# Performance work log

Measured on AMD Instinct MI355X. Metric: run time of the kernel, lower is better.

Reference implementation:

```python
import jax, jax.numpy as jnp
import numpy as np

B, T, N, DIN, DR, DH, K = 8, 40, 1024, 16, 64, 64, 3
DT = 0.05
N_EULER = 2  # Euler sub-steps per observation interval (time_points per step)


def dconv(A, x, W, b):
    feats = [x]
    h = x
    for _ in range(K - 1):
        h = jnp.einsum('bnm,bmd->bnd', A, h)
        feats.append(h)
    return jnp.concatenate(feats, -1) @ W + b


def dcgru(x, h, A, Wg, bg, Wc, bc):
    g = jax.nn.sigmoid(dconv(A, jnp.concatenate([x, h], -1), Wg, bg))
    r, u = jnp.split(g, 2, -1)
    c = jnp.tanh(dconv(A, jnp.concatenate([x, r * h], -1), Wc, bc))
    return u * h + (1.0 - u) * c


def ode_f(h, A, W0, b0, Wout, bout):
    return jnp.tanh(jnp.tanh(dconv(A, h, W0, b0)) @ Wout + bout)


def setup_inputs() -> dict:
    key = jax.random.key(0)
    ks = jax.random.split(key, 32)
    p = lambda k, s: 0.1 * jax.random.normal(k, s, dtype=jnp.float32)
    values = jax.random.normal(ks[0], (B, T, N, DIN), dtype=jnp.float32)
    masks = (jax.random.uniform(ks[1], (B, T, N, DIN)) > 0.3).astype(jnp.float32)
    u = jax.random.uniform(ks[2], (B, N, N), dtype=jnp.float32)
    A = u / u.sum(-1, keepdims=True)  # row-normalized dense diffusion matrix
    d = dict(values=values, masks=masks, A=A,
             h0=p(ks[3], (1, 1, DR)) * 0.1, z0=p(ks[4], (1, 1, DR)) * 0.1,
             gV_Wg=p(ks[5], ((DIN + DR) * K, 2 * DR)), gV_bg=jnp.zeros((2 * DR,)),
             gV_Wc=p(ks[6], ((DIN + DR) * K, DR)), gV_bc=jnp.zeros((DR,)),
             gG_Wg=p(ks[7], ((DIN + DR) * K, 2 * DR)), gG_bg=jnp.zeros((2 * DR,)),
             gG_Wc=p(ks[8], ((DIN + DR) * K, DR)), gG_bc=jnp.zeros((DR,)),
             oV_W0=p(ks[9], (DR * K, DH)), oV_b0=jnp.zeros((DH,)),
             oV_Wout=p(ks[10], (DH, DR)), oV_bout=jnp.zeros((DR,)),
             oG_W0=p(ks[11], (DR * K, DH)), oG_b0=jnp.zeros((DH,)),
             oG_Wout=p(ks[12], (DH, DR)), oG_bout=jnp.zeros((DR,)),
             Wz1=p(ks[13], (DR, DR)), bz1=jnp.zeros((DR,)),
             Wz2=p(ks[14], (DR, DR)), bz2=jnp.zeros((DR,)),
             Wz3=p(ks[15], (DR, DR)), bz3=jnp.zeros((DR,)),
             Wo=p(ks[16], (DR, DIN)), bo=jnp.zeros((DIN,)))
    return d


def reference(values, masks, A, h0, z0,
              gV_Wg, gV_bg, gV_Wc, gV_bc, gG_Wg, gG_bg, gG_Wc, gG_bc,
              oV_W0, oV_b0, oV_Wout, oV_bout, oG_W0, oG_b0, oG_Wout, oG_bout,
              Wz1, bz1, Wz2, bz2, Wz3, bz3, Wo, bo):
    X = values * masks  # [B,T,N,DIN]
    obs = (jnp.abs(masks).sum(-1, keepdims=True) > 1e-4).astype(values.dtype)  # [B,T,N,1]
    hv = jnp.broadcast_to(h0, (B, N, DR))
    zv = jnp.broadcast_to(z0, (B, N, DR))
    dt = DT / N_EULER

    def step(carry, inp):
        hv, zv = carry
        x, m = inp  # [B,N,DIN], [B,N,1]
        for _ in range(N_EULER):  # Euler ODE integration over the interval
            hv = hv + dt * ode_f(hv, A, oV_W0, oV_b0, oV_Wout, oV_bout)
            zv = zv + dt * ode_f(zv, A, oG_W0, oG_b0, oG_Wout, oG_bout)
        hv1, zv1 = hv, zv
        hv2 = dcgru(x, hv1, A, gV_Wg, gV_bg, gV_Wc, gV_bc)
        zv2 = dcgru(x, zv1, A, gG_Wg, gG_bg, gG_Wc, gG_bc)
        hv_new = hv1 * (1.0 - m) + hv2 * m
        zv_new = zv1 * (1.0 - m) + zv2 * m
        return (hv_new, zv_new), (hv1, zv1, hv_new)

    xs = (jnp.swapaxes(X, 0, 1), jnp.swapaxes(obs, 0, 1))  # time-major
    _, (hv_pre, zv_pre, hv_post) = jax.lax.scan(step, (hv, zv), xs)
    hv_pre = jnp.swapaxes(hv_pre, 0, 1)   # [B,T,N,DR]
    zv_pre = jnp.swapaxes(zv_pre, 0, 1)
    gate = jax.nn.sigmoid(jnp.tanh(jnp.tanh(zv_pre @ Wz1 + bz1) @ Wz2 + bz2) @ Wz3 + bz3)
    X_pred = (hv_pre * gate) @ Wo + bo
    return X_pred[:, 1:, :, :]
```

## Files before the change

### kernel.cpp

```cpp
#include <hip/hip_runtime.h>
#include <math.h>


#define T_ 40

typedef __attribute__((ext_vector_type(8))) short short8;
typedef __attribute__((ext_vector_type(4))) float f32x4;

__device__ __forceinline__ float sigm(float x) { return 1.0f / (1.0f + expf(-x)); }

__device__ __forceinline__ unsigned short bfrnd(float x) {
  union { float f; unsigned int u; } v; v.f = x;
  unsigned int u = v.u + 0x7fffu + ((v.u >> 16) & 1u);
  return (unsigned short)(u >> 16);
}
__device__ __forceinline__ unsigned int pk2(float a, float b) {
  return (unsigned int)bfrnd(a) | ((unsigned int)bfrnd(b) << 16);
}

__global__ __launch_bounds__(256) void k_init(float* __restrict__ S, unsigned short* __restrict__ SB,
                                              const float* __restrict__ h0,
                                              const float* __restrict__ z0) {
  int idx = blockIdx.x * 256 + threadIdx.x;
  int c = idx & 63;
  float v = (idx < (8192 * 64)) ? h0[c] : z0[c];
  S[idx] = v;
  int cc = (idx >> 10) & 63;
  float v2 = ((idx >> 16) < 8) ? h0[cc] : z0[cc];
  SB[idx] = bfrnd(v2);
}

__global__ __launch_bounds__(256) void k_asA(const float* __restrict__ A, unsigned short* __restrict__ AS) {
  size_t j = ((size_t)blockIdx.x * 256 + threadIdx.x) * 8;
  if (j >= (size_t)8 * 1024 * 1024) return;
  int b = (int)(j >> 20);
  size_t rem = j & 1048575;
  int r = (int)(rem >> 10), k = (int)(rem & 1023);
  const float* src = A + ((size_t)b << 20) + (size_t)r * 1024 + k;
  float4 v0 = *(const float4*)src;
  float4 v1 = *(const float4*)(src + 4);
  uint4 o;
  o.x = pk2(v0.x, v0.y); o.y = pk2(v0.z, v0.w);
  o.z = pk2(v1.x, v1.y); o.w = pk2(v1.z, v1.w);
  *(uint4*)(AS + ((size_t)b * 2048 + r) * 1024 + k) = o;
}

__global__ __launch_bounds__(256) void k_xb(const float* __restrict__ values,
                                            const float* __restrict__ masks,
                                            unsigned short* __restrict__ XB) {
  const int bt = blockIdx.x;
  const int n0 = blockIdx.y * 256;
  __shared__ float Ls[256][17];
  const int tid = threadIdx.x;
  size_t base = ((size_t)bt * 1024 + n0 + tid) * 16;
#pragma unroll
  for (int c4 = 0; c4 < 4; ++c4) {
    float4 v = *(const float4*)&values[base + c4 * 4];
    float4 m = *(const float4*)&masks[base + c4 * 4];
    Ls[tid][c4 * 4 + 0] = v.x * m.x; Ls[tid][c4 * 4 + 1] = v.y * m.y;
// ... 30 lines not shown

  for (int k0 = 0; k0 < 1024; k0 += 8) {
    int mm = threadIdx.x >> 1, k4 = (threadIdx.x & 1) * 4;
    float4 va = *(const float4*)&Ab[(size_t)(m0 + mm) * 1024 + k0 + k4];
    As[k4 + 0][mm] = va.x; As[k4 + 1][mm] = va.y; As[k4 + 2][mm] = va.z; As[k4 + 3][mm] = va.w;
    int kk = threadIdx.x >> 5, nn = (threadIdx.x & 31) * 4;
    float4 vb = *(const float4*)&Ab[(size_t)(k0 + kk) * 1024 + n0 + nn];
    *(float4*)&Bs[kk][nn] = vb;
    __syncthreads();
#pragma unroll
    for (int k = 0; k < 8; ++k) {
      float a[8], bb[8];
      *(float4*)&a[0] = *(float4*)&As[k][ty * 8];
      *(float4*)&a[4] = *(float4*)&As[k][ty * 8 + 4];
      *(float4*)&bb[0] = *(float4*)&Bs[k][tx * 8];
      *(float4*)&bb[4] = *(float4*)&Bs[k][tx * 8 + 4];
#pragma unroll
      for (int m = 0; m < 8; ++m)
#pragma unroll
        for (int n = 0; n < 8; ++n) acc[m][n] += a[m] * bb[n];
    }
    __syncthreads();
  }
#pragma unroll
  for (int m = 0; m < 8; ++m) {
    unsigned short* C = AS + ((size_t)b * 2048 + 1024 + m0 + ty * 8 + m) * 1024 + n0 + tx * 8;
    uint4 o;
    o.x = pk2(acc[m][0], acc[m][1]); o.y = pk2(acc[m][2], acc[m][3]);
    o.z = pk2(acc[m][4], acc[m][5]); o.w = pk2(acc[m][6], acc[m][7]);
    *(uint4*)C = o;
  }
}

template <int NT, int MODE>
__global__ __launch_bounds__(256) void k_hop_mfma(
    const unsigned short* __restrict__ AS,
    const unsigned short* __restrict__ XB,
    const unsigned short* __restrict__ SB,
    const unsigned short* __restrict__ RHB,
    float* __restrict__ HHS, float* __restrict__ HHX, int t) {
  __shared__ __align__(16) unsigned short lds_a[2][4][512];
  __shared__ __align__(16) unsigned short lds_b[2][NT][512];
  const int tid = threadIdx.x;
  const int w = tid >> 6, l = tid & 63;
  const int b = blockIdx.y;
  const int m0 = blockIdx.x * 64;
  const int lr = l & 15, lk = l >> 4;

  const unsigned short* agp = AS + ((size_t)b * 2048 + m0 + w * 16 + lr) * 1024 + lk * 8;

  const int bstart = (NT == 9) ? ((w == 0) ? 0 : (1 + 2 * w)) : (2 * w);
  const int bcnt   = (NT == 9) ? ((w == 0) ? 3 : 2) : 2;

  auto bsrc = [&](int ct) -> const unsigned short* {
    if (MODE == 1) {
      if (ct == 0)      return XB + (((size_t)(b * T_ + t)) * 16 + lr) * 1024;
      else if (ct < 5)  return SB + ((size_t)b * 64 + (size_t)(ct - 1) * 16 + lr) * 1024;
      else              return SB + ((size_t)(8 + b) * 64 + (size_t)(ct - 5) * 16 + lr) * 1024;
    } else {
      const unsigned short* base = (MODE == 2) ? RHB : SB;
      if (ct < 4) return base + ((size_t)b * 64 + (size_t)ct * 16 + lr) * 1024;
      else        return base + ((size_t)(8 + b) * 64 + (size_t)(ct - 4) * 16 + lr) * 1024;
    }
  };

  f32x4 acc[4][3];
#pragma unroll
  for (int rt = 0; rt < 4; ++rt)
#pragma unroll
    for (int ci = 0; ci < 3; ++ci) acc[rt][ci] = (f32x4){0.f, 0.f, 0.f, 0.f};

#define STAGE(BUF, K0)                                                                         \
  {                                                                                            \
    __builtin_amdgcn_global_load_lds(                                                          \
        (const __attribute__((address_space(1))) void*)(agp + (K0)),                           \
        (__attribute__((address_space(3))) void*)&lds_a[BUF][w][0], 16, 0, 0);                 \
    for (int ct = w; ct < NT; ct += 4)                                                         \
      __builtin_amdgcn_global_load_lds(                                                        \
          (const __attribute__((address_space(1))) void*)(bsrc(ct) + (K0) + lk * 8),           \
          (__attribute__((address_space(3))) void*)&lds_b[BUF][ct][0], 16, 0, 0);              \
  }

  int cur = 0;
  STAGE(0, 0)
  __syncthreads();
  for (int step = 0; step < 32; ++step) {
    const int nxt = cur ^ 1;
    if (step < 31) STAGE(nxt, (step + 1) * 32)
    short8 af[4];
#pragma unroll
    for (int rt = 0; rt < 4; ++rt)
      af[rt] = *(const short8*)&lds_a[cur][rt][l * 8];
#pragma unroll
    for (int ci = 0; ci < 3; ++ci) {
      if (ci < bcnt) {
        short8 bf = *(const short8*)&lds_b[cur][bstart + ci][l * 8];
#pragma unroll
        for (int rt = 0; rt < 4; ++rt)
          acc[rt][ci] = __builtin_amdgcn_mfma_f32_16x16x32_bf16(af[rt], bf, acc[rt][ci], 0, 0, 0);
      }
    }
    __syncthreads();
    cur = nxt;
  }
#undef STAGE

#pragma unroll
  for (int ci = 0; ci < 3; ++ci) {
    if (ci < bcnt) {
      const int ct = bstart + ci;
      float* dst; int ldc, csub;
      if (MODE == 1) {
        if (ct == 0)     { dst = HHX + (size_t)b * 2048 * 16;      ldc = 16; csub = lr; }
        else if (ct < 5) { dst = HHS + (size_t)b * 2048 * 64;      ldc = 64; csub = (ct - 1) * 16 + lr; }
        else             { dst = HHS + (size_t)(8 + b) * 2048 * 64; ldc = 64; csub = (ct - 5) * 16 + lr; }
      } else {
        if (ct < 4) { dst = HHS + (size_t)b * 2048 * 64;       ldc = 64; csub = ct * 16 + lr; }
        else        { dst = HHS + (size_t)(8 + b) * 2048 * 64; ldc = 64; csub = (ct - 4) * 16 + lr; }
      }
#pragma unroll
      for (int rt = 0; rt < 4; ++rt) {
        const int rbase = m0 + rt * 16 + lk * 4;
#pragma unroll
        for (int j = 0; j < 4; ++j)
          dst[(size_t)(rbase + j) * ldc + csub] = acc[rt][ci][j];
      }
    }
  }
}

__global__ __launch_bounds__(256) void k_ode_tail(float* __restrict__ S, unsigned short* __restrict__ SB,
    const float* __restrict__ HHS,
    const float* __restrict__ vW0, const float* __restrict__ vb0,
    const float* __restrict__ vWout, const float* __restrict__ vbout,
    const float* __restrict__ gW0, const float* __restrict__ gb0,
    const float* __restrict__ gWout, const float* __restrict__ gbout) {
  __shared__ float Fs[32][200];
  __shared__ float T1s[32][68];
  __shared__ float Wc[64][64];
  __shared__ float bias[64];
  __shared__ float Ts[64][33];
  const int rowbase = blockIdx.x * 32;
  const int i = rowbase >> 10, st = i >> 3;
  const float* W0 = st ? gW0 : vW0;
  const float* b0 = st ? gb0 : vb0;
  const float* Wo = st ? gWout : vWout;
  const float* bo = st ? gbout : vbout;
  const int r = threadIdx.x >> 3, q = threadIdx.x & 7;

  for (int idx = threadIdx.x; idx < 32 * 64; idx += 256) {
    int rr = idx >> 6, c = idx & 63;
    size_t g = (size_t)(rowbase + rr);
    int n = (int)(g & 1023);
    Fs[rr][c] = S[g * 64 + c];
    Fs[rr][64 + c]  = HHS[((size_t)i * 2048 + n) * 64 + c];
    Fs[rr][128 + c] = HHS[((size_t)i * 2048 + 1024 + n) * 64 + c];
  }
  if (threadIdx.x < 64) bias[threadIdx.x] = b0[threadIdx.x];

  float acc[8];
#pragma unroll
  for (int j = 0; j < 8; ++j) acc[j] = 0.0f;
  for (int kc = 0; kc < 3; ++kc) {
    __syncthreads();
    for (int idx = threadIdx.x; idx < 1024; idx += 256)
      ((float4*)Wc)[idx] = ((const float4*)W0)[kc * 1024 + idx];
    __syncthreads();
#pragma unroll 8
    for (int k = 0; k < 64; ++k) {
      float f = Fs[r][kc * 64 + k];
      float4 w0 = *(float4*)&Wc[k][q * 8];
      float4 w1 = *(float4*)&Wc[k][q * 8 + 4];
      acc[0] += f * w0.x; acc[1] += f * w0.y; acc[2] += f * w0.z; acc[3] += f * w0.w;
      acc[4] += f * w1.x; acc[5] += f * w1.y; acc[6] += f * w1.z; acc[7] += f * w1.w;
    }
  }
#pragma unroll
  for (int j = 0; j < 8; ++j) T1s[r][q * 8 + j] = tanhf(acc[j] + bias[q * 8 + j]);
  __syncthreads();
  if (threadIdx.x < 64) bias[threadIdx.x] = bo[threadIdx.x];
  for (int idx = threadIdx.x; idx < 1024; idx += 256)
    ((float4*)Wc)[idx] = ((const float4*)Wo)[idx];
  __syncthreads();
  float a2[8];
#pragma unroll
  for (int j = 0; j < 8; ++j) a2[j] = 0.0f;
#pragma unroll 8
  for (int k = 0; k < 64; ++k) {
    float f = T1s[r][k];
    float4 w0 = *(float4*)&Wc[k][q * 8];
    float4 w1 = *(float4*)&Wc[k][q * 8 + 4];
    a2[0] += f * w0.x; a2[1] += f * w0.y; a2[2] += f * w0.z; a2[3] += f * w0.w;
    a2[4] += f * w1.x; a2[5] += f * w1.y; a2[6] += f * w1.z; a2[7] += f * w1.w;
  }
  size_t g = (size_t)(rowbase + r);
#pragma unroll
  for (int j = 0; j < 8; ++j) {
    size_t o = g * 64 + q * 8 + j;
    float ns = S[o] + 0.025f * tanhf(a2[j] + bias[q * 8 + j]);
    S[o] = ns;
    Ts[q * 8 + j][r] = ns;
  }
  __syncthreads();
  {
    const int c = threadIdx.x >> 2, p = threadIdx.x & 3;
    const int n0 = rowbase & 1023;
    uint4 o;
    o.x = pk2(Ts[c][p * 8 + 0], Ts[c][p * 8 + 1]);
    o.y = pk2(Ts[c][p * 8 + 2], Ts[c][p * 8 + 3]);
    o.z = pk2(Ts[c][p * 8 + 4], Ts[c][p * 8 + 5]);
    o.w = pk2(Ts[c][p * 8 + 6], Ts[c][p * 8 + 7]);
    *(uint4*)(SB + ((size_t)i * 64 + c) * 1024 + n0 + p * 8) = o;
  }
}

__global__ __launch_bounds__(256) void k_gate_tail(const float* __restrict__ values,
    const float* __restrict__ masks, const float* __restrict__ S,
    const float* __restrict__ HHS, const float* __restrict__ HHX,
    float* __restrict__ RH, unsigned short* __restrict__ RHB, float* __restrict__ U,
    const float* __restrict__ vWg, const float* __restrict__ vbg,
    const float* __restrict__ gWg, const float* __restrict__ gbg, int t) {
  __shared__ float Fs[32][248];
  __shared__ float Wc[48][128];
  __shared__ float bgs[128];
  __shared__ float Ts[64][33];
  const int rowbase = blockIdx.x * 32;
  const int i = rowbase >> 10, st = i >> 3, b = i & 7;
  const float* Wg = st ? gWg : vWg;
  const float* bg = st ? gbg : vbg;
  const int r = threadIdx.x >> 3, q = threadIdx.x & 7;

  for (int idx = threadIdx.x; idx < 32 * 80; idx += 256) {
    int rr = idx / 80, c = idx - rr * 80;
    size_t g = (size_t)(rowbase + rr);
    int n = (int)(g & 1023);
    float xh, v1, v2;
    if (c < 16) {
      size_t xo = ((((size_t)b * T_ + t) << 10) + n) * 16 + c;
      xh = values[xo] * masks[xo];
      v1 = HHX[((size_t)b * 2048 + n) * 16 + c];
      v2 = HHX[((size_t)b * 2048 + 1024 + n) * 16 + c];
    } else {
      xh = S[g * 64 + (c - 16)];
      v1 = HHS[((size_t)i * 2048 + n) * 64 + (c - 16)];
      v2 = HHS[((size_t)i * 2048 + 1024 + n) * 64 + (c - 16)];
    }
    Fs[rr][c] = xh;
    Fs[rr][80 + c]  = v1;
    Fs[rr][160 + c] = v2;
  }
  if (threadIdx.x < 128) bgs[threadIdx.x] = bg[threadIdx.x];

  float acc[16];
#pragma unroll
  for (int j = 0; j < 16; ++j) acc[j] = 0.0f;
  for (int kc = 0; kc < 5; ++kc) {
    __syncthreads();
    for (int idx = threadIdx.x; idx < 1536; idx += 256)
      ((float4*)Wc)[idx] = ((const float4*)Wg)[kc * 1536 + idx];
    __syncthreads();
#pragma unroll 8
    for (int k = 0; k < 48; ++k) {
      float f = Fs[r][kc * 48 + k];
      float4 w0 = *(float4*)&Wc[k][q * 16];
      float4 w1 = *(float4*)&Wc[k][q * 16 + 4];
      float4 w2 = *(float4*)&Wc[k][q * 16 + 8];
      float4 w3 = *(float4*)&Wc[k][q * 16 + 12];
      acc[0]  += f * w0.x; acc[1]  += f * w0.y; acc[2]  += f * w0.z; acc[3]  += f * w0.w;
      acc[4]  += f * w1.x; acc[5]  += f * w1.y; acc[6]  += f * w1.z; acc[7]  += f * w1.w;
      acc[8]  += f * w2.x; acc[9]  += f * w2.y; acc[10] += f * w2.z; acc[11] += f * w2.w;
      acc[12] += f * w3.x; acc[13] += f * w3.y; acc[14] += f * w3.z; acc[15] += f * w3.w;
    }
  }
  size_t g = (size_t)(rowbase + r);
  if (q < 4) {
#pragma unroll
    for (int jj = 0; jj < 16; ++jj) {
      int c = q * 16 + jj;
      float rr_ = sigm(acc[jj] + bgs[c]);
      float rhv = rr_ * Fs[r][16 + c];
      RH[g * 64 + c] = rhv;
      Ts[c][r] = rhv;
    }
  } else {
#pragma unroll
    for (int jj = 0; jj < 16; ++jj) {
      int c = (q - 4) * 16 + jj;
      U[g * 64 + c] = sigm(acc[jj] + bgs[64 + c]);
    }
  }
  __syncthreads();
  {
    const int c = threadIdx.x >> 2, p = threadIdx.x & 3;
    const int n0 = rowbase & 1023;
    uint4 o;
    o.x = pk2(Ts[c][p * 8 + 0], Ts[c][p * 8 + 1]);
    o.y = pk2(Ts[c][p * 8 + 2], Ts[c][p * 8 + 3]);
    o.z = pk2(Ts[c][p * 8 + 4], Ts[c][p * 8 + 5]);
    o.w = pk2(Ts[c][p * 8 + 6], Ts[c][p * 8 + 7]);
    *(uint4*)(RHB + ((size_t)i * 64 + c) * 1024 + n0 + p * 8) = o;
  }
}

__global__ __launch_bounds__(256) void k_cand_tail(const float* __restrict__ values,
    const float* __restrict__ masks, float* __restrict__ S, unsigned short* __restrict__ SB,
    const float* __restrict__ HHS, const float* __restrict__ HHX,
    const float* __restrict__ RH, const float* __restrict__ U,
    const float* __restrict__ vWc, const float* __restrict__ vbc,
    const float* __restrict__ gWc, const float* __restrict__ gbc, int t) {
  __shared__ float Fs[32][248];
  __shared__ float Wc[48][64];
  __shared__ float bcs[64];
  __shared__ float Ms[32];
  __shared__ float Ts[64][33];
  const int rowbase = blockIdx.x * 32;
  const int i = rowbase >> 10, st = i >> 3, b = i & 7;
  const float* Wcc = st ? gWc : vWc;
  const float* bc = st ? gbc : vbc;
  const int r = threadIdx.x >> 3, q = threadIdx.x & 7;

  for (int idx = threadIdx.x; idx < 32 * 80; idx += 256) {
    int rr = idx / 80, c = idx - rr * 80;
    size_t g = (size_t)(rowbase + rr);
    int n = (int)(g & 1023);
    float xh, v1, v2;
    if (c < 16) {
      size_t xo = ((((size_t)b * T_ + t) << 10) + n) * 16 + c;
      xh = values[xo] * masks[xo];
      v1 = HHX[((size_t)b * 2048 + n) * 16 + c];
      v2 = HHX[((size_t)b * 2048 + 1024 + n) * 16 + c];
    } else {
      xh = RH[g * 64 + (c - 16)];
      v1 = HHS[((size_t)i * 2048 + n) * 64 + (c - 16)];
      v2 = HHS[((size_t)i * 2048 + 1024 + n) * 64 + (c - 16)];
    }
    Fs[rr][c] = xh;
    Fs[rr][80 + c]  = v1;
    Fs[rr][160 + c] = v2;
  }
  if (threadIdx.x < 64) bcs[threadIdx.x] = bc[threadIdx.x];
  if (threadIdx.x < 32) {
    int n = (rowbase + threadIdx.x) & 1023;
    size_t xo = ((((size_t)b * T_ + t) << 10) + n) * 16;
    float s = 0.0f;
    for (int d = 0; d < 16; ++d) s += fabsf(masks[xo + d]);
    Ms[threadIdx.x] = (s > 1e-4f) ? 1.0f : 0.0f;
  }

  float acc[8];
#pragma unroll
  for (int j = 0; j < 8; ++j) acc[j] = 0.0f;
  for (int kc = 0; kc < 5; ++kc) {
    __syncthreads();
    for (int idx = threadIdx.x; idx < 768; idx += 256)
      ((float4*)Wc)[idx] = ((const float4*)Wcc)[kc * 768 + idx];
    __syncthreads();
#pragma unroll 8
    for (int k = 0; k < 48; ++k) {
      float f = Fs[r][kc * 48 + k];
      float4 w0 = *(float4*)&Wc[k][q * 8];
      float4 w1 = *(float4*)&Wc[k][q * 8 + 4];
      acc[0] += f * w0.x; acc[1] += f * w0.y; acc[2] += f * w0.z; acc[3] += f * w0.w;
      acc[4] += f * w1.x; acc[5] += f * w1.y; acc[6] += f * w1.z; acc[7] += f * w1.w;
    }
  }
  size_t g = (size_t)(rowbase + r);
  float m = Ms[r];
#pragma unroll
  for (int jj = 0; jj < 8; ++jj) {
    int c = q * 8 + jj;
    float cc = tanhf(acc[jj] + bcs[c]);
    float h1 = S[g * 64 + c];
    float u  = U[g * 64 + c];
    float h2 = u * h1 + (1.0f - u) * cc;
    float ns = h1 * (1.0f - m) + h2 * m;
    S[g * 64 + c] = ns;
    Ts[c][r] = ns;
  }
  __syncthreads();
  {
    const int c = threadIdx.x >> 2, p = threadIdx.x & 3;
    const int n0 = rowbase & 1023;
    uint4 o;
    o.x = pk2(Ts[c][p * 8 + 0], Ts[c][p * 8 + 1]);
    o.y = pk2(Ts[c][p * 8 + 2], Ts[c][p * 8 + 3]);
    o.z = pk2(Ts[c][p * 8 + 4], Ts[c][p * 8 + 5]);
    o.w = pk2(Ts[c][p * 8 + 6], Ts[c][p * 8 + 7]);
    *(uint4*)(SB + ((size_t)i * 64 + c) * 1024 + n0 + p * 8) = o;
  }
}

__global__ __launch_bounds__(256) void k_out(const float* __restrict__ S,
    const float* __restrict__ Wz1, const float* __restrict__ bz1,
    const float* __restrict__ Wz2, const float* __restrict__ bz2,
    const float* __restrict__ Wz3, const float* __restrict__ bz3,
    const float* __restrict__ Wo, const float* __restrict__ bo,
    float* __restrict__ out, int t) {
  __shared__ float Zs[32][68];
  __shared__ float T1s[32][68];
  __shared__ float Hs[32][68];
  __shared__ float Wc[64][64];
  __shared__ float bias[64];
  const int rowbase = blockIdx.x * 32;
  const int r = threadIdx.x >> 3, q = threadIdx.x & 7;

  for (int idx = threadIdx.x; idx < 2048; idx += 256) {
    int rr = idx >> 6, c = idx & 63;
    size_t g = (size_t)(rowbase + rr);
    Zs[rr][c] = S[(size_t)524288 + g * 64 + c];
    Hs[rr][c] = S[g * 64 + c];
  }

#define LAYER(SRC, DST, WPTR, BPTR, ACT)                                            \
  __syncthreads();                                                                  \
  for (int idx = threadIdx.x; idx < 1024; idx += 256)                               \
    ((float4*)Wc)[idx] = ((const float4*)(WPTR))[idx];                              \
  if (threadIdx.x < 64) bias[threadIdx.x] = (BPTR)[threadIdx.x];                    \
  __syncthreads();                                                                  \
  {                                                                                 \
    float ac[8] = {0, 0, 0, 0, 0, 0, 0, 0};                                         \
    _Pragma("unroll 8") for (int k = 0; k < 64; ++k) {                              \
// ... 37 lines not shown
                              void* d_out, int out_size, void* d_ws, size_t ws_size,
                              hipStream_t stream) {
  const float* values = (const float*)d_in[0];
  const float* masks  = (const float*)d_in[1];
  const float* A      = (const float*)d_in[2];
  const float* h0     = (const float*)d_in[3];
  const float* z0     = (const float*)d_in[4];
  const float* gV_Wg  = (const float*)d_in[5];
  const float* gV_bg  = (const float*)d_in[6];
  const float* gV_Wc  = (const float*)d_in[7];
  const float* gV_bc  = (const float*)d_in[8];
  const float* gG_Wg  = (const float*)d_in[9];
  const float* gG_bg  = (const float*)d_in[10];
  const float* gG_Wc  = (const float*)d_in[11];
  const float* gG_bc  = (const float*)d_in[12];
  const float* oV_W0  = (const float*)d_in[13];
  const float* oV_b0  = (const float*)d_in[14];
  const float* oV_Wout = (const float*)d_in[15];
  const float* oV_bout = (const float*)d_in[16];
  const float* oG_W0  = (const float*)d_in[17];
  const float* oG_b0  = (const float*)d_in[18];
  const float* oG_Wout = (const float*)d_in[19];
  const float* oG_bout = (const float*)d_in[20];
  const float* Wz1 = (const float*)d_in[21];
  const float* bz1 = (const float*)d_in[22];
  const float* Wz2 = (const float*)d_in[23];
  const float* bz2 = (const float*)d_in[24];
  const float* Wz3 = (const float*)d_in[25];
  const float* bz3 = (const float*)d_in[26];
  const float* Wo  = (const float*)d_in[27];
  const float* bo  = (const float*)d_in[28];
  float* out = (float*)d_out;

  if (ws_size < (size_t)70254592) return;
  char* ws = (char*)d_ws;
  float* S            = (float*)(ws + 0);
  float* RH           = (float*)(ws + 4194304);
  float* U            = (float*)(ws + 8388608);
  float* HHS          = (float*)(ws + 12582912);
  float* HHX          = (float*)(ws + 20971520);
  unsigned short* SB  = (unsigned short*)(ws + 22020096);
  unsigned short* RHB = (unsigned short*)(ws + 24117248);
  unsigned short* XB  = (unsigned short*)(ws + 26214400);
  unsigned short* AS  = (unsigned short*)(ws + 36700160);

  k_asA<<<4096, 256, 0, stream>>>(A, AS);
  k_a2<<<dim3(8, 8, 8), 256, 0, stream>>>(A, AS);
  k_init<<<4096, 256, 0, stream>>>(S, SB, h0, z0);
  k_xb<<<dim3(320, 4), 256, 0, stream>>>(values, masks, XB);

  for (int t = 0; t < T_; ++t) {
    for (int e = 0; e < 2; ++e) {
      k_hop_mfma<8, 0><<<dim3(32, 8), 256, 0, stream>>>(AS, XB, SB, RHB, HHS, HHX, t);
      k_ode_tail<<<512, 256, 0, stream>>>(S, SB, HHS, oV_W0, oV_b0, oV_Wout, oV_bout,
                                          oG_W0, oG_b0, oG_Wout, oG_bout);
    }
    if (t >= 1)
      k_out<<<256, 256, 0, stream>>>(S, Wz1, bz1, Wz2, bz2, Wz3, bz3, Wo, bo, out, t);
    k_hop_mfma<9, 1><<<dim3(32, 8), 256, 0, stream>>>(AS, XB, SB, RHB, HHS, HHX, t);
    k_gate_tail<<<512, 256, 0, stream>>>(values, masks, S, HHS, HHX, RH, RHB, U,
                                         gV_Wg, gV_bg, gG_Wg, gG_bg, t);
    k_hop_mfma<8, 2><<<dim3(32, 8), 256, 0, stream>>>(AS, XB, SB, RHB, HHS, HHX, t);
    k_cand_tail<<<512, 256, 0, stream>>>(values, masks, S, SB, HHS, HHX, RH, U,
                                         gV_Wc, gV_bc, gG_Wc, gG_bc, t);
  }
}
```

Measured before the change: 9.470 ms.

## Fuse diffusion-hop MFMA kernels with their dense tails and ping-pong state buffers

Merges each hop-matmul kernel with its following dense/activation tail into one kernel per stage. Each block now owns 16 nodes and keeps the hop results in LDS instead of writing the HHS/HHX intermediates to global memory. The bf16 state buffer is double-buffered so blocks can update it while other blocks still read the old copy. It also skips the GRU stages at the last time step, whose results are never output. In exchange each block does less MFMA work on smaller tiles, uses more LDS, runs the tail GEMV redundantly per block, and uses a 64x8 grid.

```diff
diff --git a/kernel.cpp b/kernel.cpp
--- a/kernel.cpp
+++ b/kernel.cpp
@@ -23,8 +23,7 @@
                                               const float* __restrict__ z0) {
   int idx = blockIdx.x * 256 + threadIdx.x;
   int c = idx & 63;
-  float v = (idx < (8192 * 64)) ? h0[c] : z0[c];
-  S[idx] = v;
+  S[idx] = (idx < (8192 * 64)) ? h0[c] : z0[c];
   int cc = (idx >> 10) & 63;
   float v2 = ((idx >> 16) < 8) ? h0[cc] : z0[cc];
   SB[idx] = bfrnd(v2);
@@ -121,53 +120,121 @@
   }
 }
 
-template <int NT, int MODE>
-__global__ __launch_bounds__(256) void k_hop_mfma(
+template <int MODE>
+__global__ __launch_bounds__(256) void k_fused(
     const unsigned short* __restrict__ AS,
     const unsigned short* __restrict__ XB,
-    const unsigned short* __restrict__ SB,
-    const unsigned short* __restrict__ RHB,
-    float* __restrict__ HHS, float* __restrict__ HHX, int t) {
-  __shared__ __align__(16) unsigned short lds_a[2][4][512];
-  __shared__ __align__(16) unsigned short lds_b[2][NT][512];
+    const unsigned short* __restrict__ SBr,
+    unsigned short* __restrict__ SBw,
+    const unsigned short* __restrict__ RHBin,
+    unsigned short* __restrict__ RHBout,
+    float* __restrict__ S, float* __restrict__ RH, float* __restrict__ U,
+    const float* __restrict__ values, const float* __restrict__ masks,
+    const float* __restrict__ W1h, const float* __restrict__ b1h,
+    const float* __restrict__ W2h, const float* __restrict__ b2h,
+    const float* __restrict__ W1z, const float* __restrict__ b1z,
+    const float* __restrict__ W2z, const float* __restrict__ b2z,
+    int t) {
+  constexpr int NT = (MODE == 0) ? 8 : 9;
+  constexpr int KF = (MODE == 0) ? 192 : 240;
+  constexpr int FW = KF + 1;
+  constexpr int NTILE = 2 + NT;
+  constexpr int CHK = (MODE == 0) ? 64 : 48;
+  constexpr int CW = (MODE == 1) ? 128 : 64;
+  constexpr int CWP = CW + 4;
+  constexpr int NCHK = KF / CHK;
+  constexpr int R0_STAGE = 2 * NTILE * 1024;
+  constexpr int R0_W = CHK * CWP * 4 + ((MODE == 0) ? 16 * 68 * 4 : 0);
+  constexpr int R0 = (R0_STAGE > R0_W) ? R0_STAGE : R0_W;
+
+  __shared__ __align__(16) char r0[R0];
+  __shared__ float feats[2][16][FW];
+  __shared__ float Ts[2][64][17];
+  __shared__ float Ms[16];
+
+  unsigned short* stg = (unsigned short*)r0;
+  float* Wcs = (float*)r0;
+  float* T1 = (float*)(r0 + 64 * 68 * 4);
+
   const int tid = threadIdx.x;
   const int w = tid >> 6, l = tid & 63;
+  const int lr = l & 15, lk = l >> 4;
   const int b = blockIdx.y;
-  const int m0 = blockIdx.x * 64;
-  const int lr = l & 15, lk = l >> 4;
-
-  const unsigned short* agp = AS + ((size_t)b * 2048 + m0 + w * 16 + lr) * 1024 + lk * 8;
-
-  const int bstart = (NT == 9) ? ((w == 0) ? 0 : (1 + 2 * w)) : (2 * w);
-  const int bcnt   = (NT == 9) ? ((w == 0) ? 3 : 2) : 2;
-
-  auto bsrc = [&](int ct) -> const unsigned short* {
-    if (MODE == 1) {
-      if (ct == 0)      return XB + (((size_t)(b * T_ + t)) * 16 + lr) * 1024;
-      else if (ct < 5)  return SB + ((size_t)b * 64 + (size_t)(ct - 1) * 16 + lr) * 1024;
-      else              return SB + ((size_t)(8 + b) * 64 + (size_t)(ct - 5) * 16 + lr) * 1024;
+  const int n0 = blockIdx.x * 16;
+
+  const unsigned short* ag =
+      AS + ((size_t)b * 2048 + (w == 1 ? 1024 : 0) + n0 + lr) * 1024 + lk * 8;
+
+  auto tsrc = [&](int ct) -> const unsigned short* {
+    if (MODE == 0) {
+      int st = ct >> 2, cl = ct & 3;
+      return SBr + ((size_t)(st * 8 + b) * 64 + cl * 16 + lr) * 1024 + lk * 8;
     } else {
-      const unsigned short* base = (MODE == 2) ? RHB : SB;
-      if (ct < 4) return base + ((size_t)b * 64 + (size_t)ct * 16 + lr) * 1024;
-      else        return base + ((size_t)(8 + b) * 64 + (size_t)(ct - 4) * 16 + lr) * 1024;
+      if (ct == 0) return XB + ((size_t)(b * T_ + t) * 16 + lr) * 1024 + lk * 8;
+      const unsigned short* base = (MODE == 1) ? SBr : RHBin;
+      int st = (ct <= 4) ? 0 : 1;
+      int cl = (ct <= 4) ? (ct - 1) : (ct - 5);
+      return base + ((size_t)(st * 8 + b) * 64 + cl * 16 + lr) * 1024 + lk * 8;
     }
   };
-
-  f32x4 acc[4][3];
-#pragma unroll
-  for (int rt = 0; rt < 4; ++rt)
+  const unsigned short* bs0 = tsrc(w);
+  const unsigned short* bs1 = tsrc(w + 4);
+  const unsigned short* bs2 = (NT == 9 && w == 0) ? tsrc(8) : bs0;
+  const int bcnt = (NT == 9 && w == 0) ? 3 : 2;
+
+  if (MODE == 0) {
+    for (int idx = tid; idx < 512; idx += 256) {
+      int st = idx >> 8, rr = (idx >> 4) & 15, c4 = idx & 15;
+      float4 v = *(const float4*)&S[((size_t)(st * 8 + b) * 1024 + n0 + rr) * 64 + c4 * 4];
+      feats[st][rr][c4 * 4 + 0] = v.x; feats[st][rr][c4 * 4 + 1] = v.y;
+      feats[st][rr][c4 * 4 + 2] = v.z; feats[st][rr][c4 * 4 + 3] = v.w;
+    }
+  } else {
+    for (int idx = tid; idx < 64; idx += 256) {
+      int rr = idx >> 2, c4 = idx & 3;
+      size_t xo = ((size_t)(b * T_ + t) * 1024 + n0 + rr) * 16 + c4 * 4;
+      float4 v = *(const float4*)&values[xo];
+      float4 m = *(const float4*)&masks[xo];
+      float xv[4] = {v.x * m.x, v.y * m.y, v.z * m.z, v.w * m.w};
+#pragma unroll
+      for (int j = 0; j < 4; ++j) {
+        feats[0][rr][c4 * 4 + j] = xv[j];
+        feats[1][rr][c4 * 4 + j] = xv[j];
+      }
+    }
+    const float* bp = (MODE == 1) ? S : RH;
+    for (int idx = tid; idx < 512; idx += 256) {
+      int st = idx >> 8, rr = (idx >> 4) & 15, c4 = idx & 15;
+      float4 v = *(const float4*)&bp[((size_t)(st * 8 + b) * 1024 + n0 + rr) * 64 + c4 * 4];
+      feats[st][rr][16 + c4 * 4 + 0] = v.x; feats[st][rr][16 + c4 * 4 + 1] = v.y;
+      feats[st][rr][16 + c4 * 4 + 2] = v.z; feats[st][rr][16 + c4 * 4 + 3] = v.w;
+    }
+  }
+  if (MODE == 2 && tid < 16) {
+    int n = n0 + tid;
+    size_t xo = ((size_t)(b * T_ + t) * 1024 + n) * 16;
+    float s = 0.0f;
+    for (int d = 0; d < 16; ++d) s += fabsf(masks[xo + d]);
+    Ms[tid] = (s > 1e-4f) ? 1.0f : 0.0f;
+  }
+
+  f32x4 acc[2][3];
+#pragma unroll
+  for (int rt = 0; rt < 2; ++rt)
 #pragma unroll
     for (int ci = 0; ci < 3; ++ci) acc[rt][ci] = (f32x4){0.f, 0.f, 0.f, 0.f};
 
-#define STAGE(BUF, K0)                                                                         \
-  {                                                                                            \
-    __builtin_amdgcn_global_load_lds(                                                          \
-        (const __attribute__((address_space(1))) void*)(agp + (K0)),                           \
-        (__attribute__((address_space(3))) void*)&lds_a[BUF][w][0], 16, 0, 0);                 \
-    for (int ct = w; ct < NT; ct += 4)                                                         \
-      __builtin_amdgcn_global_load_lds(                                                        \
-          (const __attribute__((address_space(1))) void*)(bsrc(ct) + (K0) + lk * 8),           \
-          (__attribute__((address_space(3))) void*)&lds_b[BUF][ct][0], 16, 0, 0);              \
+#define GLD(SRC, SLOT, BUF)                                                                   \
+  __builtin_amdgcn_global_load_lds(                                                           \
+      (const __attribute__((address_space(1))) void*)(SRC),                                   \
+      (__attribute__((address_space(3))) void*)(stg + ((BUF)*NTILE + (SLOT)) * 512), 16, 0, 0)
+
+#define STAGE(BUF, K0)                                                                        \
+  {                                                                                           \
+    if (w < 2) GLD(ag + (K0), w, BUF);                                                        \
+    GLD(bs0 + (K0), 2 + w, BUF);                                                              \
+    GLD(bs1 + (K0), 2 + w + 4, BUF);                                                          \
+    if (NT == 9 && w == 0) GLD(bs2 + (K0), 2 + 8, BUF);                                       \
   }
 
   int cur = 0;
@@ -176,306 +243,186 @@
   for (int step = 0; step < 32; ++step) {
     const int nxt = cur ^ 1;
     if (step < 31) STAGE(nxt, (step + 1) * 32)
-    short8 af[4];
-#pragma unroll
-    for (int rt = 0; rt < 4; ++rt)
-      af[rt] = *(const short8*)&lds_a[cur][rt][l * 8];
-#pragma unroll
-    for (int ci = 0; ci < 3; ++ci) {
-      if (ci < bcnt) {
-        short8 bf = *(const short8*)&lds_b[cur][bstart + ci][l * 8];
-#pragma unroll
-        for (int rt = 0; rt < 4; ++rt)
-          acc[rt][ci] = __builtin_amdgcn_mfma_f32_16x16x32_bf16(af[rt], bf, acc[rt][ci], 0, 0, 0);
-      }
+    short8 a0f = *(const short8*)&stg[(cur * NTILE + 0) * 512 + l * 8];
+    short8 a1f = *(const short8*)&stg[(cur * NTILE + 1) * 512 + l * 8];
+    short8 b0f = *(const short8*)&stg[(cur * NTILE + 2 + w) * 512 + l * 8];
+    short8 b1f = *(const short8*)&stg[(cur * NTILE + 2 + w + 4) * 512 + l * 8];
+    acc[0][0] = __builtin_amdgcn_mfma_f32_16x16x32_bf16(a0f, b0f, acc[0][0], 0, 0, 0);
+    acc[1][0] = __builtin_amdgcn_mfma_f32_16x16x32_bf16(a1f, b0f, acc[1][0], 0, 0, 0);
+    acc[0][1] = __builtin_amdgcn_mfma_f32_16x16x32_bf16(a0f, b1f, acc[0][1], 0, 0, 0);
+    acc[1][1] = __builtin_amdgcn_mfma_f32_16x16x32_bf16(a1f, b1f, acc[1][1], 0, 0, 0);
+    if (NT == 9 && w == 0) {
+      short8 b2f = *(const short8*)&stg[(cur * NTILE + 2 + 8) * 512 + l * 8];
+      acc[0][2] = __builtin_amdgcn_mfma_f32_16x16x32_bf16(a0f, b2f, acc[0][2], 0, 0, 0);
+      acc[1][2] = __builtin_amdgcn_mfma_f32_16x16x32_bf16(a1f, b2f, acc[1][2], 0, 0, 0);
     }
     __syncthreads();
     cur = nxt;
   }
 #undef STAGE
+#undef GLD
 
 #pragma unroll
   for (int ci = 0; ci < 3; ++ci) {
     if (ci < bcnt) {
-      const int ct = bstart + ci;
-      float* dst; int ldc, csub;
-      if (MODE == 1) {
-        if (ct == 0)     { dst = HHX + (size_t)b * 2048 * 16;      ldc = 16; csub = lr; }
-        else if (ct < 5) { dst = HHS + (size_t)b * 2048 * 64;      ldc = 64; csub = (ct - 1) * 16 + lr; }
-        else             { dst = HHS + (size_t)(8 + b) * 2048 * 64; ldc = 64; csub = (ct - 5) * 16 + lr; }
+      const int ct = w + ci * 4;
+#pragma unroll
+      for (int rt = 0; rt < 2; ++rt) {
+#pragma unroll
+        for (int j = 0; j < 4; ++j) {
+          float v = acc[rt][ci][j];
+          int row = lk * 4 + j;
+          if (MODE == 0) {
+            int st = ct >> 2;
+            feats[st][row][64 + rt * 64 + (ct & 3) * 16 + lr] = v;
+          } else {
+            if (ct == 0) {
+              int col = 80 + rt * 80 + lr;
+              feats[0][row][col] = v;
+              feats[1][row][col] = v;
+            } else {
+              int st = (ct <= 4) ? 0 : 1;
+              int cl = (ct <= 4) ? (ct - 1) : (ct - 5);
+              feats[st][row][80 + rt * 80 + 16 + cl * 16 + lr] = v;
+            }
+          }
+        }
+      }
+    }
+  }
+  __syncthreads();
+
+  const int r_ = tid >> 4, cq = tid & 15;
+
+  if (MODE == 0) {
+    for (int st = 0; st < 2; ++st) {
+      const float* W1 = st ? W1z : W1h;
+      const float* B1 = st ? b1z : b1h;
+      const float* W2 = st ? W2z : W2h;
+      const float* B2 = st ? b2z : b2h;
+      float a4[4] = {0, 0, 0, 0};
+      for (int kc = 0; kc < NCHK; ++kc) {
+        __syncthreads();
+        for (int idx = tid; idx < 1024; idx += 256) {
+          int k = idx >> 4, c4 = idx & 15;
+          *(float4*)&Wcs[k * 68 + c4 * 4] = *(const float4*)&W1[(size_t)(kc * 64 + k) * 64 + c4 * 4];
+        }
+        __syncthreads();
+#pragma unroll 8
+        for (int k = 0; k < 64; ++k) {
+          float f = feats[st][r_][kc * 64 + k];
+          float4 w4 = *(float4*)&Wcs[k * 68 + cq * 4];
+          a4[0] += f * w4.x; a4[1] += f * w4.y; a4[2] += f * w4.z; a4[3] += f * w4.w;
+        }
+      }
+#pragma unroll
+      for (int j = 0; j < 4; ++j) T1[r_ * 68 + cq * 4 + j] = tanhf(a4[j] + B1[cq * 4 + j]);
+      __syncthreads();
+      for (int idx = tid; idx < 1024; idx += 256) {
+        int k = idx >> 4, c4 = idx & 15;
+        *(float4*)&Wcs[k * 68 + c4 * 4] = *(const float4*)&W2[(size_t)k * 64 + c4 * 4];
+      }
+      __syncthreads();
+      float o4[4] = {0, 0, 0, 0};
+#pragma unroll 8
+      for (int k = 0; k < 64; ++k) {
+        float f = T1[r_ * 68 + k];
+        float4 w4 = *(float4*)&Wcs[k * 68 + cq * 4];
+        o4[0] += f * w4.x; o4[1] += f * w4.y; o4[2] += f * w4.z; o4[3] += f * w4.w;
+      }
+      size_t g = ((size_t)(st * 8 + b) * 1024 + n0 + r_) * 64 + cq * 4;
+#pragma unroll
+      for (int j = 0; j < 4; ++j) {
+        float ns = S[g + j] + 0.025f * tanhf(o4[j] + B2[cq * 4 + j]);
+        S[g + j] = ns;
+        Ts[st][cq * 4 + j][r_] = ns;
+      }
+      __syncthreads();
+    }
+  } else if (MODE == 1) {
+    for (int st = 0; st < 2; ++st) {
+      const float* W1 = st ? W1z : W1h;
+      const float* B1 = st ? b1z : b1h;
+      float a8[8] = {0, 0, 0, 0, 0, 0, 0, 0};
+      for (int kc = 0; kc < NCHK; ++kc) {
+        __syncthreads();
+        for (int idx = tid; idx < 1536; idx += 256) {
+          int k = idx >> 5, c4 = idx & 31;
+          *(float4*)&Wcs[k * 132 + c4 * 4] = *(const float4*)&W1[(size_t)(kc * 48 + k) * 128 + c4 * 4];
+        }
+        __syncthreads();
+#pragma unroll 8
+        for (int k = 0; k < 48; ++k) {
+          float f = feats[st][r_][kc * 48 + k];
+          float4 wA = *(float4*)&Wcs[k * 132 + cq * 8];
+          float4 wB = *(float4*)&Wcs[k * 132 + cq * 8 + 4];
+          a8[0] += f * wA.x; a8[1] += f * wA.y; a8[2] += f * wA.z; a8[3] += f * wA.w;
+          a8[4] += f * wB.x; a8[5] += f * wB.y; a8[6] += f * wB.z; a8[7] += f * wB.w;
+        }
+      }
+      size_t g = ((size_t)(st * 8 + b) * 1024 + n0 + r_) * 64;
+      if (cq < 8) {
+#pragma unroll
+        for (int j = 0; j < 8; ++j) {
+          int c = cq * 8 + j;
+          float rr = sigm(a8[j] + B1[c]);
+          float rhv = rr * feats[st][r_][16 + c];
+          RH[g + c] = rhv;
+          Ts[st][c][r_] = rhv;
+        }
       } else {
-        if (ct < 4) { dst = HHS + (size_t)b * 2048 * 64;       ldc = 64; csub = ct * 16 + lr; }
-        else        { dst = HHS + (size_t)(8 + b) * 2048 * 64; ldc = 64; csub = (ct - 4) * 16 + lr; }
-      }
-#pragma unroll
-      for (int rt = 0; rt < 4; ++rt) {
-        const int rbase = m0 + rt * 16 + lk * 4;
-#pragma unroll
-        for (int j = 0; j < 4; ++j)
-          dst[(size_t)(rbase + j) * ldc + csub] = acc[rt][ci][j];
-      }
-    }
-  }
-}
-
-__global__ __launch_bounds__(256) void k_ode_tail(float* __restrict__ S, unsigned short* __restrict__ SB,
-    const float* __restrict__ HHS,
-    const float* __restrict__ vW0, const float* __restrict__ vb0,
-    const float* __restrict__ vWout, const float* __restrict__ vbout,
-    const float* __restrict__ gW0, const float* __restrict__ gb0,
-    const float* __restrict__ gWout, const float* __restrict__ gbout) {
-  __shared__ float Fs[32][200];
-  __shared__ float T1s[32][68];
-  __shared__ float Wc[64][64];
-  __shared__ float bias[64];
-  __shared__ float Ts[64][33];
-  const int rowbase = blockIdx.x * 32;
-  const int i = rowbase >> 10, st = i >> 3;
-  const float* W0 = st ? gW0 : vW0;
-  const float* b0 = st ? gb0 : vb0;
-  const float* Wo = st ? gWout : vWout;
-  const float* bo = st ? gbout : vbout;
-  const int r = threadIdx.x >> 3, q = threadIdx.x & 7;
-
-  for (int idx = threadIdx.x; idx < 32 * 64; idx += 256) {
-    int rr = idx >> 6, c = idx & 63;
-    size_t g = (size_t)(rowbase + rr);
-    int n = (int)(g & 1023);
-    Fs[rr][c] = S[g * 64 + c];
-    Fs[rr][64 + c]  = HHS[((size_t)i * 2048 + n) * 64 + c];
-    Fs[rr][128 + c] = HHS[((size_t)i * 2048 + 1024 + n) * 64 + c];
-  }
-  if (threadIdx.x < 64) bias[threadIdx.x] = b0[threadIdx.x];
-
-  float acc[8];
-#pragma unroll
-  for (int j = 0; j < 8; ++j) acc[j] = 0.0f;
-  for (int kc = 0; kc < 3; ++kc) {
-    __syncthreads();
-    for (int idx = threadIdx.x; idx < 1024; idx += 256)
-      ((float4*)Wc)[idx] = ((const float4*)W0)[kc * 1024 + idx];
-    __syncthreads();
+#pragma unroll
+        for (int j = 0; j < 8; ++j) {
+          int c = (cq - 8) * 8 + j;
+          U[g + c] = sigm(a8[j] + B1[64 + c]);
+        }
+      }
+      __syncthreads();
+    }
+  } else {
+    for (int st = 0; st < 2; ++st) {
+      const float* W1 = st ? W1z : W1h;
+      const float* B1 = st ? b1z : b1h;
+      float a4[4] = {0, 0, 0, 0};
+      for (int kc = 0; kc < NCHK; ++kc) {
+        __syncthreads();
+        for (int idx = tid; idx < 768; idx += 256) {
+          int k = idx >> 4, c4 = idx & 15;
+          *(float4*)&Wcs[k * 68 + c4 * 4] = *(const float4*)&W1[(size_t)(kc * 48 + k) * 64 + c4 * 4];
+        }
+        __syncthreads();
 #pragma unroll 8
-    for (int k = 0; k < 64; ++k) {
-      float f = Fs[r][kc * 64 + k];
-      float4 w0 = *(float4*)&Wc[k][q * 8];
-      float4 w1 = *(float4*)&Wc[k][q * 8 + 4];
-      acc[0] += f * w0.x; acc[1] += f * w0.y; acc[2] += f * w0.z; acc[3] += f * w0.w;
-      acc[4] += f * w1.x; acc[5] += f * w1.y; acc[6] += f * w1.z; acc[7] += f * w1.w;
-    }
-  }
-#pragma unroll
-  for (int j = 0; j < 8; ++j) T1s[r][q * 8 + j] = tanhf(acc[j] + bias[q * 8 + j]);
-  __syncthreads();
-  if (threadIdx.x < 64) bias[threadIdx.x] = bo[threadIdx.x];
-  for (int idx = threadIdx.x; idx < 1024; idx += 256)
-    ((float4*)Wc)[idx] = ((const float4*)Wo)[idx];
-  __syncthreads();
-  float a2[8];
-#pragma unroll
-  for (int j = 0; j < 8; ++j) a2[j] = 0.0f;
-#pragma unroll 8
-  for (int k = 0; k < 64; ++k) {
-    float f = T1s[r][k];
-    float4 w0 = *(float4*)&Wc[k][q * 8];
-    float4 w1 = *(float4*)&Wc[k][q * 8 + 4];
-    a2[0] += f * w0.x; a2[1] += f * w0.y; a2[2] += f * w0.z; a2[3] += f * w0.w;
-    a2[4] += f * w1.x; a2[5] += f * w1.y; a2[6] += f * w1.z; a2[7] += f * w1.w;
-  }
-  size_t g = (size_t)(rowbase + r);
-#pragma unroll
-  for (int j = 0; j < 8; ++j) {
-    size_t o = g * 64 + q * 8 + j;
-    float ns = S[o] + 0.025f * tanhf(a2[j] + bias[q * 8 + j]);
-    S[o] = ns;
-    Ts[q * 8 + j][r] = ns;
-  }
-  __syncthreads();
+        for (int k = 0; k < 48; ++k) {
+          float f = feats[st][r_][kc * 48 + k];
+          float4 w4 = *(float4*)&Wcs[k * 68 + cq * 4];
+          a4[0] += f * w4.x; a4[1] += f * w4.y; a4[2] += f * w4.z; a4[3] += f * w4.w;
+        }
+      }
+      size_t g = ((size_t)(st * 8 + b) * 1024 + n0 + r_) * 64;
+      float m = Ms[r_];
+#pragma unroll
+      for (int j = 0; j < 4; ++j) {
+        int c = cq * 4 + j;
+        float cc = tanhf(a4[j] + B1[c]);
+        float h1 = S[g + c];
+        float u = U[g + c];
+        float h2 = u * h1 + (1.0f - u) * cc;
+        float ns = h1 * (1.0f - m) + h2 * m;
+        S[g + c] = ns;
+        Ts[st][c][r_] = ns;
+      }
+      __syncthreads();
+    }
+  }
+
   {
-    const int c = threadIdx.x >> 2, p = threadIdx.x & 3;
-    const int n0 = rowbase & 1023;
+    unsigned short* dstbuf = (MODE == 1) ? RHBout : SBw;
+    int st = tid >> 7, c = (tid >> 1) & 63, p = tid & 1;
+    float* tp = &Ts[st][c][p * 8];
     uint4 o;
-    o.x = pk2(Ts[c][p * 8 + 0], Ts[c][p * 8 + 1]);
-    o.y = pk2(Ts[c][p * 8 + 2], Ts[c][p * 8 + 3]);
-    o.z = pk2(Ts[c][p * 8 + 4], Ts[c][p * 8 + 5]);
-    o.w = pk2(Ts[c][p * 8 + 6], Ts[c][p * 8 + 7]);
-    *(uint4*)(SB + ((size_t)i * 64 + c) * 1024 + n0 + p * 8) = o;
-  }
-}
-
-__global__ __launch_bounds__(256) void k_gate_tail(const float* __restrict__ values,
-    const float* __restrict__ masks, const float* __restrict__ S,
-    const float* __restrict__ HHS, const float* __restrict__ HHX,
-    float* __restrict__ RH, unsigned short* __restrict__ RHB, float* __restrict__ U,
-    const float* __restrict__ vWg, const float* __restrict__ vbg,
-    const float* __restrict__ gWg, const float* __restrict__ gbg, int t) {
-  __shared__ float Fs[32][248];
-  __shared__ float Wc[48][128];
-  __shared__ float bgs[128];
-  __shared__ float Ts[64][33];
-  const int rowbase = blockIdx.x * 32;
-  const int i = rowbase >> 10, st = i >> 3, b = i & 7;
-  const float* Wg = st ? gWg : vWg;
-  const float* bg = st ? gbg : vbg;
-  const int r = threadIdx.x >> 3, q = threadIdx.x & 7;
-
-  for (int idx = threadIdx.x; idx < 32 * 80; idx += 256) {
-    int rr = idx / 80, c = idx - rr * 80;
-    size_t g = (size_t)(rowbase + rr);
-    int n = (int)(g & 1023);
-    float xh, v1, v2;
-    if (c < 16) {
-      size_t xo = ((((size_t)b * T_ + t) << 10) + n) * 16 + c;
-      xh = values[xo] * masks[xo];
-      v1 = HHX[((size_t)b * 2048 + n) * 16 + c];
-      v2 = HHX[((size_t)b * 2048 + 1024 + n) * 16 + c];
-    } else {
-      xh = S[g * 64 + (c - 16)];
-      v1 = HHS[((size_t)i * 2048 + n) * 64 + (c - 16)];
-      v2 = HHS[((size_t)i * 2048 + 1024 + n) * 64 + (c - 16)];
-    }
-    Fs[rr][c] = xh;
-    Fs[rr][80 + c]  = v1;
-    Fs[rr][160 + c] = v2;
-  }
-  if (threadIdx.x < 128) bgs[threadIdx.x] = bg[threadIdx.x];
-
-  float acc[16];
-#pragma unroll
-  for (int j = 0; j < 16; ++j) acc[j] = 0.0f;
-  for (int kc = 0; kc < 5; ++kc) {
-    __syncthreads();
-    for (int idx = threadIdx.x; idx < 1536; idx += 256)
-      ((float4*)Wc)[idx] = ((const float4*)Wg)[kc * 1536 + idx];
-    __syncthreads();
-#pragma unroll 8
-    for (int k = 0; k < 48; ++k) {
-      float f = Fs[r][kc * 48 + k];
-      float4 w0 = *(float4*)&Wc[k][q * 16];
-      float4 w1 = *(float4*)&Wc[k][q * 16 + 4];
-      float4 w2 = *(float4*)&Wc[k][q * 16 + 8];
-      float4 w3 = *(float4*)&Wc[k][q * 16 + 12];
-      acc[0]  += f * w0.x; acc[1]  += f * w0.y; acc[2]  += f * w0.z; acc[3]  += f * w0.w;
-      acc[4]  += f * w1.x; acc[5]  += f * w1.y; acc[6]  += f * w1.z; acc[7]  += f * w1.w;
-      acc[8]  += f * w2.x; acc[9]  += f * w2.y; acc[10] += f * w2.z; acc[11] += f * w2.w;
-      acc[12] += f * w3.x; acc[13] += f * w3.y; acc[14] += f * w3.z; acc[15] += f * w3.w;
-    }
-  }
-  size_t g = (size_t)(rowbase + r);
-  if (q < 4) {
-#pragma unroll
-    for (int jj = 0; jj < 16; ++jj) {
-      int c = q * 16 + jj;
-      float rr_ = sigm(acc[jj] + bgs[c]);
-      float rhv = rr_ * Fs[r][16 + c];
-      RH[g * 64 + c] = rhv;
-      Ts[c][r] = rhv;
-    }
-  } else {
-#pragma unroll
-    for (int jj = 0; jj < 16; ++jj) {
-      int c = (q - 4) * 16 + jj;
-      U[g * 64 + c] = sigm(acc[jj] + bgs[64 + c]);
-    }
-  }
-  __syncthreads();
-  {
-    const int c = threadIdx.x >> 2, p = threadIdx.x & 3;
-    const int n0 = rowbase & 1023;
-    uint4 o;
-    o.x = pk2(Ts[c][p * 8 + 0], Ts[c][p * 8 + 1]);
-    o.y = pk2(Ts[c][p * 8 + 2], Ts[c][p * 8 + 3]);
-    o.z = pk2(Ts[c][p * 8 + 4], Ts[c][p * 8 + 5]);
-    o.w = pk2(Ts[c][p * 8 + 6], Ts[c][p * 8 + 7]);
-    *(uint4*)(RHB + ((size_t)i * 64 + c) * 1024 + n0 + p * 8) = o;
-  }
-}
-
-__global__ __launch_bounds__(256) void k_cand_tail(const float* __restrict__ values,
-    const float* __restrict__ masks, float* __restrict__ S, unsigned short* __restrict__ SB,
-    const float* __restrict__ HHS, const float* __restrict__ HHX,
-    const float* __restrict__ RH, const float* __restrict__ U,
-    const float* __restrict__ vWc, const float* __restrict__ vbc,
-    const float* __restrict__ gWc, const float* __restrict__ gbc, int t) {
-  __shared__ float Fs[32][248];
-  __shared__ float Wc[48][64];
-  __shared__ float bcs[64];
-  __shared__ float Ms[32];
-  __shared__ float Ts[64][33];
-  const int rowbase = blockIdx.x * 32;
-  const int i = rowbase >> 10, st = i >> 3, b = i & 7;
-  const float* Wcc = st ? gWc : vWc;
-  const float* bc = st ? gbc : vbc;
-  const int r = threadIdx.x >> 3, q = threadIdx.x & 7;
-
-  for (int idx = threadIdx.x; idx < 32 * 80; idx += 256) {
-    int rr = idx / 80, c = idx - rr * 80;
-    size_t g = (size_t)(rowbase + rr);
-    int n = (int)(g & 1023);
-    float xh, v1, v2;
-    if (c < 16) {
-      size_t xo = ((((size_t)b * T_ + t) << 10) + n) * 16 + c;
-      xh = values[xo] * masks[xo];
-      v1 = HHX[((size_t)b * 2048 + n) * 16 + c];
-      v2 = HHX[((size_t)b * 2048 + 1024 + n) * 16 + c];
-    } else {
-      xh = RH[g * 64 + (c - 16)];
-      v1 = HHS[((size_t)i * 2048 + n) * 64 + (c - 16)];
-      v2 = HHS[((size_t)i * 2048 + 1024 + n) * 64 + (c - 16)];
-    }
-    Fs[rr][c] = xh;
-    Fs[rr][80 + c]  = v1;
-    Fs[rr][160 + c] = v2;
-  }
-  if (threadIdx.x < 64) bcs[threadIdx.x] = bc[threadIdx.x];
-  if (threadIdx.x < 32) {
-    int n = (rowbase + threadIdx.x) & 1023;
-    size_t xo = ((((size_t)b * T_ + t) << 10) + n) * 16;
-    float s = 0.0f;
-    for (int d = 0; d < 16; ++d) s += fabsf(masks[xo + d]);
-    Ms[threadIdx.x] = (s > 1e-4f) ? 1.0f : 0.0f;
-  }
-
-  float acc[8];
-#pragma unroll
-  for (int j = 0; j < 8; ++j) acc[j] = 0.0f;
-  for (int kc = 0; kc < 5; ++kc) {
-    __syncthreads();
-    for (int idx = threadIdx.x; idx < 768; idx += 256)
-      ((float4*)Wc)[idx] = ((const float4*)Wcc)[kc * 768 + idx];
-    __syncthreads();
-#pragma unroll 8
-    for (int k = 0; k < 48; ++k) {
-      float f = Fs[r][kc * 48 + k];
-      float4 w0 = *(float4*)&Wc[k][q * 8];
-      float4 w1 = *(float4*)&Wc[k][q * 8 + 4];
-      acc[0] += f * w0.x; acc[1] += f * w0.y; acc[2] += f * w0.z; acc[3] += f * w0.w;
-      acc[4] += f * w1.x; acc[5] += f * w1.y; acc[6] += f * w1.z; acc[7] += f * w1.w;
-    }
-  }
-  size_t g = (size_t)(rowbase + r);
-  float m = Ms[r];
-#pragma unroll
-  for (int jj = 0; jj < 8; ++jj) {
-    int c = q * 8 + jj;
-    float cc = tanhf(acc[jj] + bcs[c]);
-    float h1 = S[g * 64 + c];
-    float u  = U[g * 64 + c];
-    float h2 = u * h1 + (1.0f - u) * cc;
-    float ns = h1 * (1.0f - m) + h2 * m;
-    S[g * 64 + c] = ns;
-    Ts[c][r] = ns;
-  }
-  __syncthreads();
-  {
-    const int c = threadIdx.x >> 2, p = threadIdx.x & 3;
-    const int n0 = rowbase & 1023;
-    uint4 o;
-    o.x = pk2(Ts[c][p * 8 + 0], Ts[c][p * 8 + 1]);
-    o.y = pk2(Ts[c][p * 8 + 2], Ts[c][p * 8 + 3]);
-    o.z = pk2(Ts[c][p * 8 + 4], Ts[c][p * 8 + 5]);
-    o.w = pk2(Ts[c][p * 8 + 6], Ts[c][p * 8 + 7]);
-    *(uint4*)(SB + ((size_t)i * 64 + c) * 1024 + n0 + p * 8) = o;
+    o.x = pk2(tp[0], tp[1]); o.y = pk2(tp[2], tp[3]);
+    o.z = pk2(tp[4], tp[5]); o.w = pk2(tp[6], tp[7]);
+    *(uint4*)(dstbuf + ((size_t)(st * 8 + b) * 64 + c) * 1024 + n0 + p * 8) = o;
   }
 }
 
@@ -579,36 +526,39 @@
   const float* bo  = (const float*)d_in[28];
   float* out = (float*)d_out;
 
-  if (ws_size < (size_t)70254592) return;
+  if (ws_size < (size_t)62914560) return;
   char* ws = (char*)d_ws;
   float* S            = (float*)(ws + 0);
   float* RH           = (float*)(ws + 4194304);
   float* U            = (float*)(ws + 8388608);
-  float* HHS          = (float*)(ws + 12582912);
-  float* HHX          = (float*)(ws + 20971520);
-  unsigned short* SB  = (unsigned short*)(ws + 22020096);
-  unsigned short* RHB = (unsigned short*)(ws + 24117248);
-  unsigned short* XB  = (unsigned short*)(ws + 26214400);
-  unsigned short* AS  = (unsigned short*)(ws + 36700160);
+  unsigned short* SBa = (unsigned short*)(ws + 12582912);
+  unsigned short* SBb = (unsigned short*)(ws + 14680064);
+  unsigned short* RHB = (unsigned short*)(ws + 16777216);
+  unsigned short* XB  = (unsigned short*)(ws + 18874368);
+  unsigned short* AS  = (unsigned short*)(ws + 29360128);
 
   k_asA<<<4096, 256, 0, stream>>>(A, AS);
   k_a2<<<dim3(8, 8, 8), 256, 0, stream>>>(A, AS);
-  k_init<<<4096, 256, 0, stream>>>(S, SB, h0, z0);
+  k_init<<<4096, 256, 0, stream>>>(S, SBa, h0, z0);
   k_xb<<<dim3(320, 4), 256, 0, stream>>>(values, masks, XB);
 
+  const dim3 fg(64, 8);
   for (int t = 0; t < T_; ++t) {
-    for (int e = 0; e < 2; ++e) {
-      k_hop_mfma<8, 0><<<dim3(32, 8), 256, 0, stream>>>(AS, XB, SB, RHB, HHS, HHX, t);
-      k_ode_tail<<<512, 256, 0, stream>>>(S, SB, HHS, oV_W0, oV_b0, oV_Wout, oV_bout,
-                                          oG_W0, oG_b0, oG_Wout, oG_bout);
-    }
+    k_fused<0><<<fg, 256, 0, stream>>>(AS, XB, SBa, SBb, RHB, RHB, S, RH, U, values, masks,
+                                       oV_W0, oV_b0, oV_Wout, oV_bout,
+                                       oG_W0, oG_b0, oG_Wout, oG_bout, t);
+    k_fused<0><<<fg, 256, 0, stream>>>(AS, XB, SBb, SBa, RHB, RHB, S, RH, U, values, masks,
+                                       oV_W0, oV_b0, oV_Wout, oV_bout,
+                                       oG_W0, oG_b0, oG_Wout, oG_bout, t);
     if (t >= 1)
       k_out<<<256, 256, 0, stream>>>(S, Wz1, bz1, Wz2, bz2, Wz3, bz3, Wo, bo, out, t);
-    k_hop_mfma<9, 1><<<dim3(32, 8), 256, 0, stream>>>(AS, XB, SB, RHB, HHS, HHX, t);
-    k_gate_tail<<<512, 256, 0, stream>>>(values, masks, S, HHS, HHX, RH, RHB, U,
-                                         gV_Wg, gV_bg, gG_Wg, gG_bg, t);
-    k_hop_mfma<8, 2><<<dim3(32, 8), 256, 0, stream>>>(AS, XB, SB, RHB, HHS, HHX, t);
-    k_cand_tail<<<512, 256, 0, stream>>>(values, masks, S, SB, HHS, HHX, RH, U,
-                                         gV_Wc, gV_bc, gG_Wc, gG_bc, t);
-  }
-}
+    if (t < T_ - 1) {
+      k_fused<1><<<fg, 256, 0, stream>>>(AS, XB, SBa, SBb, RHB, RHB, S, RH, U, values, masks,
+                                         gV_Wg, gV_bg, nullptr, nullptr,
+                                         gG_Wg, gG_bg, nullptr, nullptr, t);
+      k_fused<2><<<fg, 256, 0, stream>>>(AS, XB, SBa, SBa, RHB, RHB, S, RH, U, values, masks,
+                                         gV_Wc, gV_bc, nullptr, nullptr,
+                                         gG_Wc, gG_bc, nullptr, nullptr, t);
+    }
+  }
+}
```

Result: faster. 8.997 ms (-5.0%).
